# Kernel tuning notes

Measured on AMD Instinct MI355X. Metric: run time of the kernel, lower is better.

The kernel has to match this reference:

```python
import jax, jax.numpy as jnp
import numpy as np

EMBED, HIDDEN, VOCAB = 512, 512, 30000
B, S, K, NT = 16, 128, 49, 5


def _lin(x, W, b):
    # torch nn.Linear: y = x @ W.T + b, W stored as (out, in)
    return x @ W.T + b


def setup_inputs() -> dict:
    key = jax.random.key(0)
    ks = jax.random.split(key, 32)
    g = lambda i, shape, scale=0.05: (jax.random.normal(ks[i], shape, dtype=jnp.float32) * scale)
    inp = {
        "epoch": 30,
        "h_t": jax.random.normal(ks[0], (B, S, HIDDEN), dtype=jnp.float32),
        "V": jax.random.normal(ks[1], (B, K, HIDDEN), dtype=jnp.float32),
        "T": jax.random.normal(ks[2], (B, NT, EMBED), dtype=jnp.float32),
        "W_ZV": g(3, (49, HIDDEN)), "b_ZV": jnp.zeros((49,), jnp.float32),
        "W_Zh": g(4, (49, HIDDEN)), "b_Zh": jnp.zeros((49,), jnp.float32),
        "W_az": g(5, (1, 49)), "b_az": jnp.zeros((1,), jnp.float32),
        "W_QT": g(6, (5, EMBED)), "b_QT": jnp.zeros((5,), jnp.float32),
        "W_Qh": g(7, (5, HIDDEN)), "b_Qh": jnp.zeros((5,), jnp.float32),
        "W_bq": g(8, (1, 5)), "b_bq": jnp.zeros((1,), jnp.float32),
        "W_sq": g(9, (EMBED, EMBED)), "b_sq": jnp.zeros((EMBED,), jnp.float32),
        "W_sh": g(10, (EMBED, HIDDEN)), "b_sh": jnp.zeros((EMBED,), jnp.float32),
        "W_Ss": g(11, (5, EMBED)), "b_Ss": jnp.zeros((5,), jnp.float32),
        "W_Sr": g(12, (5, EMBED)), "b_Sr": jnp.zeros((5,), jnp.float32),
        "W_sz": g(13, (EMBED, HIDDEN)), "b_sz": jnp.zeros((EMBED,), jnp.float32),
        "W_mlp": g(14, (VOCAB, EMBED)), "b_mlp": jnp.zeros((VOCAB,), jnp.float32),
    }
    return inp


def reference(epoch, h_t, V, T,
              W_ZV, b_ZV, W_Zh, b_Zh, W_az, b_az,
              W_QT, b_QT, W_Qh, b_Qh, W_bq, b_bq,
              W_sq, b_sq, W_sh, b_sh, W_Ss, b_Ss,
              W_Sr, b_Sr, W_sz, b_sz, W_mlp, b_mlp):
    # --- visual attention (dropout = identity, eval mode) ---
    # content_V: [B, S, K, 49]
    content_V = _lin(V, W_ZV, b_ZV)[:, None, :, :] + _lin(h_t, W_Zh, b_Zh)[:, :, None, :]
    visual_t = (jnp.tanh(content_V) @ W_az.T + b_az)[..., 0]          # [B, S, K]
    alpha_t = jax.nn.softmax(visual_t, axis=-1)
    z_t = jnp.einsum('bsk,bkh->bsh', alpha_t, V)                      # [B, S, H]
    r_t = jnp.tanh(_lin(z_t, W_sz, b_sz))                             # [B, S, E]
    # --- topic attention ---
    content_T = _lin(T, W_QT, b_QT)[:, None, :, :] + _lin(h_t, W_Qh, b_Qh)[:, :, None, :]  # [B,S,5,5]
    topic_t = (jnp.tanh(content_T) @ W_bq.T + b_bq)[..., 0]           # [B, S, 5]
    beta_t = jax.nn.softmax(topic_t, axis=-1)
    q_t = jnp.einsum('bst,bte->bse', beta_t, T)                       # [B, S, E]
    s_t = jnp.tanh(_lin(q_t, W_sq, b_sq) + _lin(h_t, W_sh, b_sh))     # [B, S, E]
    # --- sentinel scores: the torch loop reduces to (batch 0, diagonal pos) only ---
    qh0 = _lin(h_t[0], W_Qh, b_Qh)                                    # [S, 5]
    score_s = jnp.tanh(_lin(s_t[0], W_Ss, b_Ss) + qh0) @ W_bq.T + b_bq  # [S, 1]
    score_r = jnp.tanh(_lin(r_t[0], W_Sr, b_Sr) + qh0) @ W_bq.T + b_bq  # [S, 1]
    if epoch <= 20:
        gama_t = 1.0
    else:
        gama_t = jax.nn.sigmoid(score_s - score_r)[None, :, :]        # [1, S, 1]
    c_t = gama_t * s_t + (1.0 - gama_t) * r_t                         # [B, S, E]
    scores = _lin(c_t, W_mlp, b_mlp)                                  # [B, S, vocab]
    return scores
```

## Files before the change

kernel.cpp:

```cpp
#include <hip/hip_runtime.h>
#include <hip/hip_bf16.h>


typedef short bf16x8 __attribute__((ext_vector_type(8)));
typedef float f32x4 __attribute__((ext_vector_type(4)));
typedef short short8 __attribute__((ext_vector_type(8)));

static __device__ __forceinline__ short f2bf(float f) {
    union { float f; unsigned u; } v; v.f = f;
    unsigned r = v.u + 0x7FFFu + ((v.u >> 16) & 1u);
    return (short)(r >> 16);
}

static __device__ __forceinline__ void cvt_blk(const float* __restrict__ src,
                                               short* __restrict__ dst, int i) {
    const float4 a = ((const float4*)src)[i * 2];
    const float4 b = ((const float4*)src)[i * 2 + 1];
    short8 o;
    o[0] = f2bf(a.x); o[1] = f2bf(a.y); o[2] = f2bf(a.z); o[3] = f2bf(a.w);
    o[4] = f2bf(b.x); o[5] = f2bf(b.y); o[6] = f2bf(b.z); o[7] = f2bf(b.w);
    ((short8*)dst)[i] = o;
}

#define GLD_LDS16(gp, lp)                                                          \
    __builtin_amdgcn_global_load_lds(                                              \
        (const __attribute__((address_space(1))) unsigned int*)(gp),               \
        (__attribute__((address_space(3))) unsigned int*)(lp), 16, 0, 0)

__global__ __launch_bounds__(256) void k_front(
    const float* __restrict__ h, const float* __restrict__ V, const float* __restrict__ T,
    const float* __restrict__ W_Zh, const float* __restrict__ W_Qh,
    const float* __restrict__ W_ZV, const float* __restrict__ W_QT,
    short* __restrict__ P1, short* __restrict__ P2, short* __restrict__ P3,
    short* __restrict__ V_b, short* __restrict__ T_b, short* __restrict__ h_b)
{
    const int bid = blockIdx.x;
    const int t = threadIdx.x;

    if (bid < 48) {
        const int pid = bid >> 4, blk = bid & 15;
        short* dst = (pid == 0) ? P1 : (pid == 1) ? P2 : P3;
        const int base = blk * 2048 + t * 8;
        const int r = base >> 9, c = base & 511;
        const float* srow = nullptr;
        if (pid == 0)      srow = (r < 49) ? (W_Zh + r * 512) : ((r < 54) ? (W_Qh + (r - 49) * 512) : nullptr);
        else if (pid == 1) srow = (r < 49) ? (W_ZV + r * 512) : nullptr;
        else               srow = (r < 5)  ? (W_QT + r * 512) : nullptr;
        short8 o = {0, 0, 0, 0, 0, 0, 0, 0};
        if (srow) {
            const float4 a = *(const float4*)(srow + c);
            const float4 b = *(const float4*)(srow + c + 4);
            o[0] = f2bf(a.x); o[1] = f2bf(a.y); o[2] = f2bf(a.z); o[3] = f2bf(a.w);
            o[4] = f2bf(b.x); o[5] = f2bf(b.y); o[6] = f2bf(b.z); o[7] = f2bf(b.w);
        }
        *(short8*)(dst + base) = o;
        return;
    }
    if (bid < 244)      cvt_blk(V, V_b, (bid - 48) * 256 + t);
    else if (bid < 264) cvt_blk(T, T_b, (bid - 244) * 256 + t);
    else                cvt_blk(h, h_b, (bid - 264) * 256 + t);
}

__global__ __launch_bounds__(256) void k_linhv(
    const short* __restrict__ h_b, const short* __restrict__ V_b, const short* __restrict__ T_b,
    const short* __restrict__ P1, const short* __restrict__ P2, const short* __restrict__ P3,
    const float* __restrict__ b_Zh, const float* __restrict__ b_Qh,
    const float* __restrict__ b_ZV, const float* __restrict__ b_QT,
    float* __restrict__ Zh, float* __restrict__ Qh,
    float* __restrict__ ZV, float* __restrict__ QT)
{
    constexpr int K = 512;
    const int bid = blockIdx.x;
    int sect, m0;
    const short *Ag, *Wg;
    if (bid < 32)      { sect = 0; m0 = bid * 64;        Ag = h_b; Wg = P1; }
    else if (bid < 45) { sect = 1; m0 = (bid - 32) * 64; Ag = V_b; Wg = P2; }
    else               { sect = 2; m0 = (bid - 45) * 64; Ag = T_b; Wg = P3; }

    __shared__ __align__(16) short sA[64 * 64];
    __shared__ __align__(16) short sW[64 * 64];
    const int tid = threadIdx.x;
    const int l = tid & 63, w = tid >> 6;
    const int wm = (w & 1) * 32, wn = (w >> 1) * 32;
    const int lm = l & 15, lg = l >> 4;
    const int sr = l >> 3, sc = l & 7;
    f32x4 acc[2][2] = {};

    for (int k0 = 0; k0 < K; k0 += 64) {
        #pragma unroll
        for (int c = 0; c < 2; ++c) {
            const int R = w * 16 + c * 8;
            const int row = R + sr;
            GLD_LDS16(Ag + (size_t)(m0 + row) * K + k0 + ((sc ^ (row & 7)) << 3), sA + R * 64);
            GLD_LDS16(Wg + (size_t)row * K + k0 + ((sc ^ (row & 7)) << 3), sW + R * 64);
        }
        __syncthreads();
        bf16x8 af[2][2], bv[2][2];
        #pragma unroll
        for (int s = 0; s < 2; ++s)
            #pragma unroll
            for (int i = 0; i < 2; ++i) {
                const int ra = wm + i * 16 + lm;
                const int rb = wn + i * 16 + lm;
                af[s][i] = *(const bf16x8*)(sA + ra * 64 + (((s * 4 + lg) ^ (ra & 7)) << 3));
                bv[s][i] = *(const bf16x8*)(sW + rb * 64 + (((s * 4 + lg) ^ (rb & 7)) << 3));
            }
        #pragma unroll
        for (int s = 0; s < 2; ++s)
            #pragma unroll
            for (int i = 0; i < 2; ++i)
                #pragma unroll
                for (int j = 0; j < 2; ++j)
                    acc[i][j] = __builtin_amdgcn_mfma_f32_16x16x32_bf16(af[s][i], bv[s][j], acc[i][j], 0, 0, 0);
        __syncthreads();
    }

    #pragma unroll
    for (int j = 0; j < 2; ++j) {
        const int n = wn + j * 16 + lm;
        #pragma unroll
        for (int i = 0; i < 2; ++i) {
            #pragma unroll
            for (int q = 0; q < 4; ++q) {
                const int m = m0 + wm + i * 16 + lg * 4 + q;
                const float v = acc[i][j][q];
                if (sect == 0) {
                    if (n < 49)      Zh[(size_t)m * 64 + n] = v + b_Zh[n];
                    else if (n < 54) Qh[(size_t)m * 8 + (n - 49)] = v + b_Qh[n - 49];
                } else if (sect == 1) {
                    if (m < 784 && n < 49) ZV[(size_t)m * 64 + n] = v + b_ZV[n];
                } else {
                    if (m < 80 && n < 5) QT[(size_t)m * 8 + n] = v + b_QT[n];
                }
            }
        }
    }
}

__global__ void k_attn(const float* __restrict__ V, const float* __restrict__ T,
                       const float* __restrict__ ZV, const float* __restrict__ Zh,
                       const float* __restrict__ QT, const float* __restrict__ Qh,
                       const float* __restrict__ W_az, const float* __restrict__ b_az,
                       const float* __restrict__ W_bq, const float* __restrict__ b_bq,
                       short* __restrict__ z_bf, short* __restrict__ q_bf,
                       const float* __restrict__ wsz, short* __restrict__ wsz_b,
                       const float* __restrict__ wsq, short* __restrict__ wsq_b,
                       const float* __restrict__ wsh, short* __restrict__ wsh_b,
                       const float* __restrict__ wmlp, short* __restrict__ wmlp_b)
{
    const int bid = blockIdx.x;
    const int t = threadIdx.x;
    if (bid >= 2048) {
        if (bid < 2176)      cvt_blk(wsz, wsz_b, (bid - 2048) * 256 + t);
        else if (bid < 2304) cvt_blk(wsq, wsq_b, (bid - 2176) * 256 + t);
        else if (bid < 2432) cvt_blk(wsh, wsh_b, (bid - 2304) * 256 + t);
        else                 cvt_blk(wmlp, wmlp_b, (bid - 2432) * 256 + t);
        return;
    }
    const int row = bid;
    const int b = row >> 7;
    __shared__ float zh[49], waz[49], alpha[49], beta[5];
    if (t < 49) { zh[t] = Zh[row * 64 + t]; waz[t] = W_az[t]; }
    __syncthreads();
    if (t < 49) {
        const float* zv = ZV + (b * 49 + t) * 64;
        float acc = b_az[0];
        for (int j = 0; j < 49; ++j) acc += tanhf(zv[j] + zh[j]) * waz[j];
        alpha[t] = acc;
    } else if (t >= 64 && t < 69) {
        const int tt = t - 64;
        const float* qt = QT + (b * 5 + tt) * 8;
        const float* qh = Qh + row * 8;
        float acc = b_bq[0];
        for (int j = 0; j < 5; ++j) acc += tanhf(qt[j] + qh[j]) * W_bq[j];
        beta[tt] = acc;
    }
    __syncthreads();
    const int wv = t >> 6, l = t & 63;
    if (wv == 0) {
        float a = (l < 49) ? alpha[l] : -1e30f;
        float m = a;
        #pragma unroll
        for (int off = 32; off; off >>= 1) m = fmaxf(m, __shfl_xor(m, off));
        float e = (l < 49) ? expf(a - m) : 0.f;
        float s = e;
        #pragma unroll
        for (int off = 32; off; off >>= 1) s += __shfl_xor(s, off);
        if (l < 49) alpha[l] = e / s;
    } else if (wv == 1) {
        float a = (l < 5) ? beta[l] : -1e30f;
        float m = a;
        #pragma unroll
        for (int off = 32; off; off >>= 1) m = fmaxf(m, __shfl_xor(m, off));
        float e = (l < 5) ? expf(a - m) : 0.f;
        float s = e;
        #pragma unroll
        for (int off = 32; off; off >>= 1) s += __shfl_xor(s, off);
        if (l < 5) beta[l] = e / s;
    }
    __syncthreads();
    const float* Vb = V + (size_t)b * 49 * 512;
    const float* Tb = T + (size_t)b * 5 * 512;
    for (int hd = t; hd < 512; hd += 256) {
        float az = 0.f;
        #pragma unroll
        for (int k = 0; k < 49; ++k) az = fmaf(alpha[k], Vb[k * 512 + hd], az);
        z_bf[(size_t)row * 512 + hd] = f2bf(az);
        float aq = 0.f;
        #pragma unroll
        for (int k = 0; k < 5; ++k) aq = fmaf(beta[k], Tb[k * 512 + hd], aq);
        q_bf[(size_t)row * 512 + hd] = f2bf(aq);
    }
}

__global__ __launch_bounds__(256) void k_rs(
    const short* __restrict__ Zb, const short* __restrict__ Qb, const short* __restrict__ Hb,
    const short* __restrict__ Wsz, const short* __restrict__ Wsq, const short* __restrict__ Wsh,
    const float* __restrict__ b_sz, const float* __restrict__ b_sq, const float* __restrict__ b_sh,
    float* __restrict__ r_t, float* __restrict__ s_t)
{
    constexpr int K = 512, NN = 512;
    __shared__ __align__(16) short sA[64 * 64];
    __shared__ __align__(16) short sW[64 * 64];
    const int tid = threadIdx.x;
    const int l = tid & 63, w = tid >> 6;
    const int m0 = blockIdx.x * 64, n0 = blockIdx.y * 64;
    const int wm = (w & 1) * 32, wn = (w >> 1) * 32;
    const int lm = l & 15, lg = l >> 4;
    const int sr = l >> 3, sc = l & 7;
    f32x4 accr[2][2] = {}, accs[2][2] = {};

#define RS_PASS(AG, WG, ACC)                                                      \
    for (int k0 = 0; k0 < K; k0 += 64) {                                          \
        _Pragma("unroll")                                                         \
        for (int c = 0; c < 2; ++c) {                                             \
            const int R = w * 16 + c * 8;                                         \
            const int row = R + sr;                                               \
            GLD_LDS16((AG) + (size_t)(m0 + row) * K + k0 + ((sc ^ (row & 7)) << 3), sA + R * 64); \
            GLD_LDS16((WG) + (size_t)(n0 + row) * K + k0 + ((sc ^ (row & 7)) << 3), sW + R * 64); \
        }                                                                         \
        __syncthreads();                                                          \
        bf16x8 af[2][2], bv[2][2];                                                \
        _Pragma("unroll")                                                         \
        for (int s = 0; s < 2; ++s)                                               \
            _Pragma("unroll")                                                     \
            for (int i = 0; i < 2; ++i) {                                         \
                const int ra = wm + i * 16 + lm;                                  \
                const int rb = wn + i * 16 + lm;                                  \
                af[s][i] = *(const bf16x8*)(sA + ra * 64 + (((s * 4 + lg) ^ (ra & 7)) << 3)); \
                bv[s][i] = *(const bf16x8*)(sW + rb * 64 + (((s * 4 + lg) ^ (rb & 7)) << 3)); \
            }                                                                     \
        _Pragma("unroll")                                                         \
        for (int s = 0; s < 2; ++s)                                               \
            _Pragma("unroll")                                                     \
            for (int i = 0; i < 2; ++i)                                           \
                _Pragma("unroll")                                                 \
                for (int j = 0; j < 2; ++j)                                       \
                    ACC[i][j] = __builtin_amdgcn_mfma_f32_16x16x32_bf16(af[s][i], bv[s][j], ACC[i][j], 0, 0, 0); \
        __syncthreads();                                                          \
    }

    RS_PASS(Zb, Wsz, accr)
    RS_PASS(Qb, Wsq, accs)
    RS_PASS(Hb, Wsh, accs)
#undef RS_PASS

    #pragma unroll
    for (int j = 0; j < 2; ++j) {
        const int n = n0 + wn + j * 16 + lm;
        const float br = b_sz[n];
        const float bs = b_sq[n] + b_sh[n];
        #pragma unroll
        for (int i = 0; i < 2; ++i) {
            const int m = m0 + wm + i * 16 + lg * 4;
            #pragma unroll
            for (int q = 0; q < 4; ++q) {
                r_t[(size_t)(m + q) * NN + n] = tanhf(accr[i][j][q] + br);
                s_t[(size_t)(m + q) * NN + n] = tanhf(accs[i][j][q] + bs);
            }
        }
    }
}

__global__ __launch_bounds__(256, 4) void k_gemm_mlp(
    const short* __restrict__ A, const short* __restrict__ Wb,
    const float* __restrict__ bias, float* __restrict__ C)
{
    constexpr int N = 30000, K = 512;
    __shared__ __align__(16) short shA[128 * 64];
    __shared__ __align__(16) short shW[128 * 64];
    const int tid = threadIdx.x;
    const int l = tid & 63, w = tid >> 6;
    const int bid = blockIdx.x;
    const int swz = (bid & 7) * 470 + (bid >> 3);
    const int m0 = (swz & 15) * 128;
    const int n0 = (swz >> 4) * 128;
    const int wm = (w & 1) * 64, wn = (w >> 1) * 64;
    const int lm = l & 15, lg = l >> 4;
    const int sr = tid >> 3, sc = tid & 7;
    const short* Ag = A  + (size_t)m0 * K;
    const short* Wg = Wb + (size_t)n0 * K;
    f32x4 acc[4][4] = {};

    for (int t = 0; t < 8; ++t) {
        const int kk = t * 64;
        #pragma unroll
        for (int c = 0; c < 4; ++c) {
            const int row = c * 32 + sr;
            GLD_LDS16(Ag + (size_t)row * K + kk + ((sc ^ (row & 7)) << 3),
                      &shA[(c * 32 + w * 8) * 64]);
            GLD_LDS16(Wg + (size_t)row * K + kk + ((sc ^ (row & 7)) << 3),
                      &shW[(c * 32 + w * 8) * 64]);
        }
        __syncthreads();
        bf16x8 af[2][4], bv[2][4];
        #pragma unroll
        for (int s = 0; s < 2; ++s)
            #pragma unroll
            for (int i = 0; i < 4; ++i) {
                const int ra = wm + i * 16 + lm;
                const int rb = wn + i * 16 + lm;
                const int ck = s * 4 + lg;
                af[s][i] = *(const bf16x8*)(&shA[ra * 64 + ((ck ^ (ra & 7)) << 3)]);
                bv[s][i] = *(const bf16x8*)(&shW[rb * 64 + ((ck ^ (rb & 7)) << 3)]);
            }
        #pragma unroll
        for (int s = 0; s < 2; ++s)
            #pragma unroll
            for (int i = 0; i < 4; ++i)
                #pragma unroll
                for (int j = 0; j < 4; ++j)
                    acc[i][j] = __builtin_amdgcn_mfma_f32_16x16x32_bf16(
                        af[s][i], bv[s][j], acc[i][j], 0, 0, 0);
        __syncthreads();
    }

    #pragma unroll
    for (int j = 0; j < 4; ++j) {
        const int n = n0 + wn + j * 16 + lm;
        if (n >= N) continue;
        const float bj = bias[n];
        #pragma unroll
        for (int i = 0; i < 4; ++i) {
            const int m = m0 + wm + i * 16 + lg * 4;
            #pragma unroll
            for (int q = 0; q < 4; ++q)
                __builtin_nontemporal_store(acc[i][j][q] + bj, &C[(size_t)(m + q) * N + n]);
        }
    }
}

__global__ __launch_bounds__(256) void k_blend_gate(
    const float* __restrict__ s_t, const float* __restrict__ r_t,
    const float* __restrict__ Qh,
    const float* __restrict__ W_Ss, const float* __restrict__ b_Ss,
    const float* __restrict__ W_Sr, const float* __restrict__ b_Sr,
    const float* __restrict__ W_bq, const float* __restrict__ b_bq,
    const int* __restrict__ epoch, short* __restrict__ c_bf)
{
    const int row = blockIdx.x;
    const int s = row & 127;
    const int t = threadIdx.x;
    float g = 1.0f;
    if (epoch[0] > 20) {
        const int l = t & 63;
        const int d = l * 8;
        const float4 s0 = *(const float4*)(s_t + (size_t)s * 512 + d);
        const float4 s1 = *(const float4*)(s_t + (size_t)s * 512 + d + 4);
        const float4 r0 = *(const float4*)(r_t + (size_t)s * 512 + d);
        const float4 r1 = *(const float4*)(r_t + (size_t)s * 512 + d + 4);
        float ss = b_bq[0], sr = b_bq[0];
        #pragma unroll
        for (int k = 0; k < 5; ++k) {
            const float4 w0 = *(const float4*)(W_Ss + k * 512 + d);
            const float4 w1 = *(const float4*)(W_Ss + k * 512 + d + 4);
            const float4 v0 = *(const float4*)(W_Sr + k * 512 + d);
            const float4 v1 = *(const float4*)(W_Sr + k * 512 + d + 4);
            float as = s0.x*w0.x + s0.y*w0.y + s0.z*w0.z + s0.w*w0.w
                     + s1.x*w1.x + s1.y*w1.y + s1.z*w1.z + s1.w*w1.w;
            float ar = r0.x*v0.x + r0.y*v0.y + r0.z*v0.z + r0.w*v0.w
                     + r1.x*v1.x + r1.y*v1.y + r1.z*v1.z + r1.w*v1.w;
            #pragma unroll
            for (int off = 32; off; off >>= 1) {
                as += __shfl_xor(as, off);
                ar += __shfl_xor(ar, off);
            }
            const float qh = Qh[s * 8 + k];
            ss += tanhf(as + b_Ss[k] + qh) * W_bq[k];
            sr += tanhf(ar + b_Sr[k] + qh) * W_bq[k];
        }
        g = 1.f / (1.f + expf(-(ss - sr)));
    }
    const size_t base = (size_t)row * 512;
    for (int i = t; i < 512; i += 256)
        c_bf[base + i] = f2bf(g * s_t[base + i] + (1.f - g) * r_t[base + i]);
}

extern "C" void kernel_launch(void* const* d_in, const int* in_sizes, int n_in,
                              void* d_out, int out_size, void* d_ws, size_t ws_size,
                              hipStream_t stream)
{
    const int*   epoch = (const int*)  d_in[0];
    const float* h_t   = (const float*)d_in[1];
    const float* V     = (const float*)d_in[2];
    const float* T     = (const float*)d_in[3];
    const float* W_ZV  = (const float*)d_in[4];  const float* b_ZV = (const float*)d_in[5];
    const float* W_Zh  = (const float*)d_in[6];  const float* b_Zh = (const float*)d_in[7];
    const float* W_az  = (const float*)d_in[8];  const float* b_az = (const float*)d_in[9];
    const float* W_QT  = (const float*)d_in[10]; const float* b_QT = (const float*)d_in[11];
    const float* W_Qh  = (const float*)d_in[12]; const float* b_Qh = (const float*)d_in[13];
    const float* W_bq  = (const float*)d_in[14]; const float* b_bq = (const float*)d_in[15];
    const float* W_sq  = (const float*)d_in[16]; const float* b_sq = (const float*)d_in[17];
    const float* W_sh  = (const float*)d_in[18]; const float* b_sh = (const float*)d_in[19];
    const float* W_Ss  = (const float*)d_in[20]; const float* b_Ss = (const float*)d_in[21];
    const float* W_Sr  = (const float*)d_in[22]; const float* b_Sr = (const float*)d_in[23];
    const float* W_sz  = (const float*)d_in[24]; const float* b_sz = (const float*)d_in[25];
    const float* W_mlp = (const float*)d_in[26]; const float* b_mlp= (const float*)d_in[27];

    float* out = (float*)d_out;
    float* ws  = (float*)d_ws;
    const size_t M1 = 1024 * 1024;
    float* r_t  = ws;
    float* s_t  = ws + M1;
    float* Zh   = ws + 2 * M1;
    float* ZV   = Zh + 2048 * 64;
    float* Qh   = ZV + 784 * 64;
    float* QT   = Qh + 2048 * 8;
    float* pad  = QT + 80 * 8;
    short* sreg = (short*)(pad + 128);
    short* z_bf   = sreg;
    short* q_bf   = z_bf + M1;
    short* h_bf   = q_bf + M1;
    short* c_bf   = h_bf + M1;
    short* Wsz_bf = c_bf + M1;
    short* Wsq_bf = Wsz_bf + 512 * 512;
    short* Wsh_bf = Wsq_bf + 512 * 512;
    short* V_bf   = Wsh_bf + 512 * 512;
    short* T_bf   = V_bf + 832 * 512;
    short* P1     = T_bf + 128 * 512;
    short* P2     = P1 + 64 * 512;
    short* P3     = P2 + 64 * 512;
    short* W_bf   = P3 + 64 * 512;

    k_front<<<776, 256, 0, stream>>>(h_t, V, T, W_Zh, W_Qh, W_ZV, W_QT,
                                     P1, P2, P3, V_bf, T_bf, h_bf);
    k_linhv<<<47, 256, 0, stream>>>(h_bf, V_bf, T_bf, P1, P2, P3,
                                    b_Zh, b_Qh, b_ZV, b_QT, Zh, Qh, ZV, QT);
    k_attn<<<9932, 256, 0, stream>>>(V, T, ZV, Zh, QT, Qh, W_az, b_az, W_bq, b_bq,
                                     z_bf, q_bf,
                                     W_sz, Wsz_bf, W_sq, Wsq_bf, W_sh, Wsh_bf,
                                     W_mlp, W_bf);
    k_rs<<<dim3(32, 8), 256, 0, stream>>>(z_bf, q_bf, h_bf, Wsz_bf, Wsq_bf, Wsh_bf,
                                          b_sz, b_sq, b_sh, r_t, s_t);
    k_blend_gate<<<2048, 256, 0, stream>>>(s_t, r_t, Qh, W_Ss, b_Ss, W_Sr, b_Sr,
                                           W_bq, b_bq, epoch, c_bf);
    k_gemm_mlp<<<3760, 256, 0, stream>>>(c_bf, W_bf, b_mlp, out);
}
```

Before: 177.7 us.

## Pre-swizzle blended activations into MFMA fragment layout and drop A-tile LDS staging

The blend/gate kernel now handles one row per wavefront with vectorized loads. It writes c_t in bf16 already permuted into the per-lane MFMA fragment order. The vocab GEMM then loads A fragments straight from global memory into registers and no longer stages the A tile through LDS. This halves LDS traffic and LDS footprint per block. The cost is A being re-read from global/L2 by every N-tile block, and a layout that is tightly coupled between the two kernels.

Result: slower. 199.8 us (+12.5%).

```diff
diff --git a/kernel.cpp b/kernel.cpp
--- a/kernel.cpp
+++ b/kernel.cpp
@@ -282,12 +282,74 @@
     }
 }
 
+__global__ __launch_bounds__(256) void k_blend_gate(
+    const float* __restrict__ s_t, const float* __restrict__ r_t,
+    const float* __restrict__ Qh,
+    const float* __restrict__ W_Ss, const float* __restrict__ b_Ss,
+    const float* __restrict__ W_Sr, const float* __restrict__ b_Sr,
+    const float* __restrict__ W_bq, const float* __restrict__ b_bq,
+    const int* __restrict__ epoch, short* __restrict__ c_bf)
+{
+    const int row = blockIdx.x * 4 + (threadIdx.x >> 6);
+    const int l = threadIdx.x & 63;
+    float g = 1.0f;
+    if (epoch[0] > 20) {
+        const int sg = row & 127;
+        const int d = l * 8;
+        const float4 s0 = *(const float4*)(s_t + (size_t)sg * 512 + d);
+        const float4 s1 = *(const float4*)(s_t + (size_t)sg * 512 + d + 4);
+        const float4 r0 = *(const float4*)(r_t + (size_t)sg * 512 + d);
+        const float4 r1 = *(const float4*)(r_t + (size_t)sg * 512 + d + 4);
+        float ss = b_bq[0], sr = b_bq[0];
+        #pragma unroll
+        for (int k = 0; k < 5; ++k) {
+            const float4 w0 = *(const float4*)(W_Ss + k * 512 + d);
+            const float4 w1 = *(const float4*)(W_Ss + k * 512 + d + 4);
+            const float4 v0 = *(const float4*)(W_Sr + k * 512 + d);
+            const float4 v1 = *(const float4*)(W_Sr + k * 512 + d + 4);
+            float as = s0.x*w0.x + s0.y*w0.y + s0.z*w0.z + s0.w*w0.w
+                     + s1.x*w1.x + s1.y*w1.y + s1.z*w1.z + s1.w*w1.w;
+            float ar = r0.x*v0.x + r0.y*v0.y + r0.z*v0.z + r0.w*v0.w
+                     + r1.x*v1.x + r1.y*v1.y + r1.z*v1.z + r1.w*v1.w;
+            #pragma unroll
+            for (int off = 32; off; off >>= 1) {
+                as += __shfl_xor(as, off);
+                ar += __shfl_xor(ar, off);
+            }
+            const float qh = Qh[sg * 8 + k];
+            ss += tanhf(as + b_Ss[k] + qh) * W_bq[k];
+            sr += tanhf(ar + b_Sr[k] + qh) * W_bq[k];
+        }
+        g = 1.f / (1.f + expf(-(ss - sr)));
+    }
+    const int kk = l * 8;
+    const float4 a0 = *(const float4*)(s_t + (size_t)row * 512 + kk);
+    const float4 a1 = *(const float4*)(s_t + (size_t)row * 512 + kk + 4);
+    const float4 b0 = *(const float4*)(r_t + (size_t)row * 512 + kk);
+    const float4 b1 = *(const float4*)(r_t + (size_t)row * 512 + kk + 4);
+    short8 o;
+    o[0] = f2bf(g * a0.x + (1.f - g) * b0.x);
+    o[1] = f2bf(g * a0.y + (1.f - g) * b0.y);
+    o[2] = f2bf(g * a0.z + (1.f - g) * b0.z);
+    o[3] = f2bf(g * a0.w + (1.f - g) * b0.w);
+    o[4] = f2bf(g * a1.x + (1.f - g) * b1.x);
+    o[5] = f2bf(g * a1.y + (1.f - g) * b1.y);
+    o[6] = f2bf(g * a1.z + (1.f - g) * b1.z);
+    o[7] = f2bf(g * a1.w + (1.f - g) * b1.w);
+    const int tm = row >> 7, rm = row & 127;
+    const int half = (rm >> 6) & 1, i2 = (rm >> 4) & 3, lm = rm & 15;
+    const int tk = l >> 3, cc = l & 7, s2 = cc >> 2, lg = cc & 3;
+    const int frag = half * 8 + i2 * 2 + s2;
+    const size_t off = ((size_t)(tm * 8 + tk)) * 8192
+                     + (size_t)(frag * 512 + lg * 128 + lm * 8);
+    *(short8*)(c_bf + off) = o;
+}
+
 __global__ __launch_bounds__(256, 4) void k_gemm_mlp(
-    const short* __restrict__ A, const short* __restrict__ Wb,
+    const short* __restrict__ At, const short* __restrict__ Wb,
     const float* __restrict__ bias, float* __restrict__ C)
 {
     constexpr int N = 30000, K = 512;
-    __shared__ __align__(16) short shA[128 * 64];
     __shared__ __align__(16) short shW[128 * 64];
     const int tid = threadIdx.x;
     const int l = tid & 63, w = tid >> 6;
@@ -298,8 +360,8 @@
     const int wm = (w & 1) * 64, wn = (w >> 1) * 64;
     const int lm = l & 15, lg = l >> 4;
     const int sr = tid >> 3, sc = tid & 7;
-    const short* Ag = A  + (size_t)m0 * K;
     const short* Wg = Wb + (size_t)n0 * K;
+    const short* Ab = At + (size_t)(swz & 15) * 8 * 8192 + (size_t)(w & 1) * 8 * 512 + l * 8;
     f32x4 acc[4][4] = {};
 
     for (int t = 0; t < 8; ++t) {
@@ -307,22 +369,24 @@
         #pragma unroll
         for (int c = 0; c < 4; ++c) {
             const int row = c * 32 + sr;
-            GLD_LDS16(Ag + (size_t)row * K + kk + ((sc ^ (row & 7)) << 3),
-                      &shA[(c * 32 + w * 8) * 64]);
             GLD_LDS16(Wg + (size_t)row * K + kk + ((sc ^ (row & 7)) << 3),
                       &shW[(c * 32 + w * 8) * 64]);
         }
+        bf16x8 af[2][4];
+        const short* Abt = Ab + (size_t)t * 8192;
+        #pragma unroll
+        for (int i = 0; i < 4; ++i) {
+            af[0][i] = *(const bf16x8*)(Abt + (i * 2 + 0) * 512);
+            af[1][i] = *(const bf16x8*)(Abt + (i * 2 + 1) * 512);
+        }
         __syncthreads();
-        bf16x8 af[2][4], bv[2][4];
+        bf16x8 bv[2][4];
         #pragma unroll
         for (int s = 0; s < 2; ++s)
             #pragma unroll
             for (int i = 0; i < 4; ++i) {
-                const int ra = wm + i * 16 + lm;
                 const int rb = wn + i * 16 + lm;
-                const int ck = s * 4 + lg;
-                af[s][i] = *(const bf16x8*)(&shA[ra * 64 + ((ck ^ (ra & 7)) << 3)]);
-                bv[s][i] = *(const bf16x8*)(&shW[rb * 64 + ((ck ^ (rb & 7)) << 3)]);
+                bv[s][i] = *(const bf16x8*)(&shW[rb * 64 + (((s * 4 + lg) ^ (rb & 7)) << 3)]);
             }
         #pragma unroll
         for (int s = 0; s < 2; ++s)
@@ -348,52 +412,6 @@
                 __builtin_nontemporal_store(acc[i][j][q] + bj, &C[(size_t)(m + q) * N + n]);
         }
     }
-}
-
-__global__ __launch_bounds__(256) void k_blend_gate(
-    const float* __restrict__ s_t, const float* __restrict__ r_t,
-    const float* __restrict__ Qh,
-    const float* __restrict__ W_Ss, const float* __restrict__ b_Ss,
-    const float* __restrict__ W_Sr, const float* __restrict__ b_Sr,
-    const float* __restrict__ W_bq, const float* __restrict__ b_bq,
-    const int* __restrict__ epoch, short* __restrict__ c_bf)
-{
-    const int row = blockIdx.x;
-    const int s = row & 127;
-    const int t = threadIdx.x;
-    float g = 1.0f;
-    if (epoch[0] > 20) {
-        const int l = t & 63;
-        const int d = l * 8;
-        const float4 s0 = *(const float4*)(s_t + (size_t)s * 512 + d);
-        const float4 s1 = *(const float4*)(s_t + (size_t)s * 512 + d + 4);
-        const float4 r0 = *(const float4*)(r_t + (size_t)s * 512 + d);
-        const float4 r1 = *(const float4*)(r_t + (size_t)s * 512 + d + 4);
-        float ss = b_bq[0], sr = b_bq[0];
-        #pragma unroll
-        for (int k = 0; k < 5; ++k) {
-            const float4 w0 = *(const float4*)(W_Ss + k * 512 + d);
-            const float4 w1 = *(const float4*)(W_Ss + k * 512 + d + 4);
-            const float4 v0 = *(const float4*)(W_Sr + k * 512 + d);
-            const float4 v1 = *(const float4*)(W_Sr + k * 512 + d + 4);
-            float as = s0.x*w0.x + s0.y*w0.y + s0.z*w0.z + s0.w*w0.w
-                     + s1.x*w1.x + s1.y*w1.y + s1.z*w1.z + s1.w*w1.w;
-            float ar = r0.x*v0.x + r0.y*v0.y + r0.z*v0.z + r0.w*v0.w
-                     + r1.x*v1.x + r1.y*v1.y + r1.z*v1.z + r1.w*v1.w;
-            #pragma unroll
-            for (int off = 32; off; off >>= 1) {
-                as += __shfl_xor(as, off);
-                ar += __shfl_xor(ar, off);
-            }
-            const float qh = Qh[s * 8 + k];
-            ss += tanhf(as + b_Ss[k] + qh) * W_bq[k];
-            sr += tanhf(ar + b_Sr[k] + qh) * W_bq[k];
-        }
-        g = 1.f / (1.f + expf(-(ss - sr)));
-    }
-    const size_t base = (size_t)row * 512;
-    for (int i = t; i < 512; i += 256)
-        c_bf[base + i] = f2bf(g * s_t[base + i] + (1.f - g) * r_t[base + i]);
 }
 
 extern "C" void kernel_launch(void* const* d_in, const int* in_sizes, int n_in,
@@ -452,7 +470,7 @@
                                      W_mlp, W_bf);
     k_rs<<<dim3(32, 8), 256, 0, stream>>>(z_bf, q_bf, h_bf, Wsz_bf, Wsq_bf, Wsh_bf,
                                           b_sz, b_sq, b_sh, r_t, s_t);
-    k_blend_gate<<<2048, 256, 0, stream>>>(s_t, r_t, Qh, W_Ss, b_Ss, W_Sr, b_Sr,
-                                           W_bq, b_bq, epoch, c_bf);
+    k_blend_gate<<<512, 256, 0, stream>>>(s_t, r_t, Qh, W_Ss, b_Ss, W_Sr, b_Sr,
+                                          W_bq, b_bq, epoch, c_bf);
     k_gemm_mlp<<<3760, 256, 0, stream>>>(c_bf, W_bf, b_mlp, out);
 }
```
